# Kernel optimization log

Hardware: AMD Instinct MI355X
Metric: run time of the kernel (lower is better)

Reference implementation:

```python
import jax, jax.numpy as jnp
import numpy as np

NEG = -1.0e9  # matches torch's masked_fill value
EPS = 1e-12


def setup_inputs() -> dict:
    key = jax.random.key(0)
    ks = jax.random.split(key, 8)
    B, T, S, E, H, M = 128, 512, 512, 256, 1024, 4

    def lin_w(k, fan_in, fan_out):
        lim = 1.0 / np.sqrt(fan_in)
        return jax.random.uniform(k, (fan_in, fan_out), jnp.float32, -lim, lim)

    return {
        "state": jax.random.normal(ks[0], (B, S), jnp.float32),
        "task_features": jax.random.normal(ks[1], (B, T, 5), jnp.float32),
        "nest_ids": jax.random.randint(ks[2], (B, T), 0, M),
        "task_mask": jnp.ones((B, T), jnp.bool_),
        "emb_w": lin_w(ks[3], 5, E),
        "emb_b": jnp.zeros((E,), jnp.float32),
        "w1": lin_w(ks[4], S + E, H),
        "b1": jnp.zeros((H,), jnp.float32),
        "w2": lin_w(ks[5], H, H),
        "b2": jnp.zeros((H,), jnp.float32),
        "w3": lin_w(ks[6], H, 1),
        "b3": jnp.zeros((1,), jnp.float32),
        "etas": jnp.ones((M,), jnp.float32),  # eta_buf (learn_eta=False, eta_init=1.0)
    }


def reference(state, task_features, nest_ids, task_mask,
              emb_w, emb_b, w1, b1, w2, b2, w3, b3, etas):
    B, T, _ = task_features.shape
    M = etas.shape[0]

    # per-task utilities: MLP over concat(state, task_embed)  [B,T]
    te = task_features @ emb_w + emb_b                                # [B,T,E]
    x = jnp.concatenate(
        [jnp.broadcast_to(state[:, None, :], (B, T, state.shape[-1])), te], axis=-1)
    h = jax.nn.relu(x @ w1 + b1)
    h = jax.nn.relu(h @ w2 + b2)
    utils = (h @ w3 + b3)[..., 0]                                     # [B,T]
    utils = jnp.where(task_mask, utils, NEG)

    # nest membership masks (vectorized segment-softmax over nests)
    mem = (nest_ids[..., None] == jnp.arange(M)) & task_mask[..., None]  # [B,T,M]
    nonempty = mem.any(axis=1)                                           # [B,M]

    mval = jnp.max(jnp.where(mem, utils[..., None], -jnp.inf), axis=1)   # [B,M]
    mval = jnp.where(nonempty, mval, 0.0)
    scaled = (utils[..., None] - mval[:, None, :]) / etas                # [B,T,M]
    sums = jnp.sum(jnp.where(mem, jnp.exp(scaled), 0.0), axis=1)         # [B,M]

    # inclusive values U_m = mval + eta_m * log(sum exp((v-mval)/eta_m))
    U = jnp.where(nonempty, mval + etas * jnp.log(jnp.clip(sums, EPS)), NEG)
    p_nest = jax.nn.softmax(U, axis=-1)                                  # [B,M]

    # per-task within-nest probabilities, gathered via nest id
    nid = jnp.clip(nest_ids, 0, M - 1)
    m_t = jnp.take_along_axis(mval, nid, axis=1)                         # [B,T]
    s_t = jnp.take_along_axis(jnp.clip(sums, EPS), nid, axis=1)          # [B,T]
    pn_t = jnp.take_along_axis(p_nest, nid, axis=1)                      # [B,T]
    e_t = jnp.exp((utils - m_t) / etas[nid])
    valid = task_mask & (nest_ids >= 0) & (nest_ids < M)
    p_task = jnp.where(valid, pn_t * e_t / s_t, 0.0)                     # [B,T]

    # degenerate fallback: uniform over valid tasks when everything underflowed
    any_valid = task_mask.any(axis=1)
    fallback = any_valid & (p_task.sum(axis=1) <= EPS)
    uni = 1.0 / jnp.maximum(task_mask.sum(axis=1), 1).astype(p_task.dtype)
    p_task = jnp.where(fallback[:, None] & task_mask, uni[:, None], p_task)

    return utils, p_task, p_nest
```

## Files before the change

### kernel.cpp

```cpp
#include <hip/hip_runtime.h>
#include <stdint.h>

#define NEGV -1.0e9f
#define EPSV 1e-12f

typedef __attribute__((ext_vector_type(8))) short bf16x8;
typedef __attribute__((ext_vector_type(4))) float f32x4;

__device__ __forceinline__ unsigned int f2bf(float f) {
  unsigned int u = __builtin_bit_cast(unsigned int, f);
  u = u + 0x7FFFu + ((u >> 16) & 1u);
  return u >> 16;
}

__device__ __forceinline__ unsigned int cvt_pk_bf16(float lo, float hi) {
  unsigned int r;
  asm("v_cvt_pk_bf16_f32 %0, %1, %2" : "=v"(r) : "v"(lo), "v"(hi));
  return r;
}

__global__ __launch_bounds__(256) void k_prep(
    const float* __restrict__ state, const float* __restrict__ w1,
    const float* __restrict__ b1, const float* __restrict__ emb_w,
    const float* __restrict__ emb_b, const float* __restrict__ w2,
    float* __restrict__ W1e, float* __restrict__ sb,
    unsigned short* __restrict__ W2t) {
  const int blk = blockIdx.x;
  const int tid = threadIdx.x;
  if (blk < 4) {
    const int j = blk * 256 + tid;
    float a0 = 0.f, a1 = 0.f, a2 = 0.f, a3 = 0.f, a4 = 0.f;
    for (int e = 0; e < 256; ++e) {
      const float w = w1[(size_t)(512 + e) * 1024 + j];
      a0 += emb_w[0 * 256 + e] * w;
      a1 += emb_w[1 * 256 + e] * w;
      a2 += emb_w[2 * 256 + e] * w;
      a3 += emb_w[3 * 256 + e] * w;
      a4 += emb_w[4 * 256 + e] * w;
    }
    W1e[0 * 1024 + j] = a0;
    W1e[1 * 1024 + j] = a1;
    W1e[2 * 1024 + j] = a2;
    W1e[3 * 1024 + j] = a3;
    W1e[4 * 1024 + j] = a4;
  } else if (blk < 516) {
    const int blk2 = blk - 4;
    const int b = blk2 >> 2;
    const int j = (blk2 & 3) * 256 + tid;
    float acc = b1[j];
    for (int e = 0; e < 256; ++e)
      acc += emb_b[e] * w1[(size_t)(512 + e) * 1024 + j];
    const float* st = state + (size_t)b * 512;
    for (int s = 0; s < 512; ++s) acc += st[s] * w1[(size_t)s * 1024 + j];
    sb[(size_t)b * 1024 + j] = acc;
  } else {
    __shared__ float tile[64][65];
    const int blk2 = blk - 516;
    const int gn = blk2 & 15, gk = blk2 >> 4;
    const int c = tid & 63, w = tid >> 6;
#pragma unroll
    for (int i = 0; i < 16; ++i) {
      const int r = i * 4 + w;
      tile[r][c] = w2[(size_t)(gk * 64 + r) * 1024 + gn * 64 + c];
    }
    __syncthreads();
#pragma unroll
    for (int i = 0; i < 16; ++i) {
      const int r = i * 4 + w;
      W2t[(size_t)(gn * 64 + r) * 1024 + gk * 64 + c] = (unsigned short)f2bf(tile[c][r]);
    }
  }
}

__global__ __launch_bounds__(256) void k_h1(
    const float* __restrict__ tf, const float* __restrict__ sbm,
    const float* __restrict__ W1em, unsigned short* __restrict__ H1) {
  const int tid = threadIdx.x;
  const int j0 = (tid & 127) << 3;
  const int r0 = (blockIdx.x * 2 + (tid >> 7)) * 8;
  const int b = r0 >> 9;
  float ptf[8][5];
#pragma unroll
  for (int r = 0; r < 8; ++r) {
    const float* f = tf + (size_t)(r0 + r) * 5;
#pragma unroll
    for (int i = 0; i < 5; ++i) ptf[r][i] = f[i];
  }
  const float* sbp = sbm + (size_t)b * 1024 + j0;
  const float4 sa = *(const float4*)(sbp);
  const float4 sbv = *(const float4*)(sbp + 4);
  float4 wa[5], wb[5];
#pragma unroll
  for (int i = 0; i < 5; ++i) {
    wa[i] = *(const float4*)(W1em + i * 1024 + j0);
    wb[i] = *(const float4*)(W1em + i * 1024 + j0 + 4);
  }
#pragma unroll
  for (int r = 0; r < 8; ++r) {
    const float f0 = ptf[r][0], f1 = ptf[r][1], f2 = ptf[r][2],
                f3 = ptf[r][3], f4 = ptf[r][4];
    float h0 = fmaf(f4, wa[4].x, fmaf(f3, wa[3].x, fmaf(f2, wa[2].x, fmaf(f1, wa[1].x, fmaf(f0, wa[0].x, sa.x)))));
    float h1 = fmaf(f4, wa[4].y, fmaf(f3, wa[3].y, fmaf(f2, wa[2].y, fmaf(f1, wa[1].y, fmaf(f0, wa[0].y, sa.y)))));
    float h2 = fmaf(f4, wa[4].z, fmaf(f3, wa[3].z, fmaf(f2, wa[2].z, fmaf(f1, wa[1].z, fmaf(f0, wa[0].z, sa.z)))));
    float h3 = fmaf(f4, wa[4].w, fmaf(f3, wa[3].w, fmaf(f2, wa[2].w, fmaf(f1, wa[1].w, fmaf(f0, wa[0].w, sa.w)))));
    float h4 = fmaf(f4, wb[4].x, fmaf(f3, wb[3].x, fmaf(f2, wb[2].x, fmaf(f1, wb[1].x, fmaf(f0, wb[0].x, sbv.x)))));
    float h5 = fmaf(f4, wb[4].y, fmaf(f3, wb[3].y, fmaf(f2, wb[2].y, fmaf(f1, wb[1].y, fmaf(f0, wb[0].y, sbv.y)))));
    float h6 = fmaf(f4, wb[4].z, fmaf(f3, wb[3].z, fmaf(f2, wb[2].z, fmaf(f1, wb[1].z, fmaf(f0, wb[0].z, sbv.z)))));
    float h7 = fmaf(f4, wb[4].w, fmaf(f3, wb[3].w, fmaf(f2, wb[2].w, fmaf(f1, wb[1].w, fmaf(f0, wb[0].w, sbv.w)))));
    h0 = fmaxf(h0, 0.f); h1 = fmaxf(h1, 0.f); h2 = fmaxf(h2, 0.f); h3 = fmaxf(h3, 0.f);
    h4 = fmaxf(h4, 0.f); h5 = fmaxf(h5, 0.f); h6 = fmaxf(h6, 0.f); h7 = fmaxf(h7, 0.f);
    uint4 pk;
    pk.x = cvt_pk_bf16(h0, h1);
    pk.y = cvt_pk_bf16(h2, h3);
    pk.z = cvt_pk_bf16(h4, h5);
    pk.w = cvt_pk_bf16(h6, h7);
    *(uint4*)&H1[(size_t)(r0 + r) * 1024 + j0] = pk;
  }
}

__global__ __launch_bounds__(512, 2) void k_gemm2(
    const unsigned short* __restrict__ H1, const unsigned short* __restrict__ W2t,
    const float* __restrict__ b2, const float* __restrict__ w3,
    float* __restrict__ partial) {
  __shared__ unsigned short As[2][16384];
  __shared__ unsigned short Bs[2][16384];

  const int bid = blockIdx.x;
  const int swz = (bid & 7) * 128 + (bid >> 3);
  const int bx = swz >> 2, by = swz & 3;
  const int row0 = bx << 8, col0 = by << 8;

  const int tid = threadIdx.x, lane = tid & 63, wid = tid >> 6;

  const int sr = (wid << 5) + (lane >> 3);
  const int scol = (((lane & 7) ^ ((lane >> 3) & 7)) << 3);
  const size_t abase = (size_t)(row0 + sr) * 1024 + scol;
  const size_t bbase = (size_t)(col0 + sr) * 1024 + scol;
  const int ldsb = (wid << 5) * 64;

#define STAGE8(kt, d)                                                         \
    _Pragma("unroll")                                                         \
    for (int q = 0; q < 4; ++q) {                                             \
      __builtin_amdgcn_global_load_lds(                                       \
          (const __attribute__((address_space(1))) void*)(                    \
              H1 + abase + (size_t)q * 8192 + (kt) * 64),                     \
          (__attribute__((address_space(3))) void*)(As[d] + ldsb + q * 512),  \
          16, 0, 0);                                                          \
      __builtin_amdgcn_global_load_lds(                                       \
          (const __attribute__((address_space(1))) void*)(                    \
              W2t + bbase + (size_t)q * 8192 + (kt) * 64),                    \
          (__attribute__((address_space(3))) void*)(Bs[d] + ldsb + q * 512),  \
          16, 0, 0);                                                          \
    }

#define STAGE4(kt, d, g)                                                      \
    _Pragma("unroll")                                                         \
    for (int qq = 2 * (g); qq < 2 * (g) + 2; ++qq) {                          \
      __builtin_amdgcn_global_load_lds(                                       \
          (const __attribute__((address_space(1))) void*)(                    \
              H1 + abase + (size_t)qq * 8192 + (kt) * 64),                    \
          (__attribute__((address_space(3))) void*)(As[d] + ldsb + qq * 512), \
          16, 0, 0);                                                          \
      __builtin_amdgcn_global_load_lds(                                       \
          (const __attribute__((address_space(1))) void*)(                    \
              W2t + bbase + (size_t)qq * 8192 + (kt) * 64),                   \
          (__attribute__((address_space(3))) void*)(Bs[d] + ldsb + qq * 512), \
          16, 0, 0);                                                          \
    }

  const int wr = wid >> 2, wc = wid & 3;
  const int lm = lane & 15, lg = lane >> 4;
  const int aoff = (wr * 128 + lm) * 64;
  const int boff = (wc * 64 + lm) * 64;
  const int s0 = ((lg ^ (lm & 7)) << 3);
  const int s1 = (((4 + lg) ^ (lm & 7)) << 3);

  f32x4 acc[8][4];
#pragma unroll
  for (int m = 0; m < 8; ++m)
#pragma unroll
    for (int n = 0; n < 4; ++n) acc[m][n] = (f32x4){0.f, 0.f, 0.f, 0.f};

  STAGE8(0, 0);
  __syncthreads();

#pragma unroll 1
  for (int t = 0; t < 16; ++t) {
    const unsigned short* Ad = As[t & 1];
    const unsigned short* Bd = Bs[t & 1];
    bf16x8 bk0[4], bk1[4], aS[2][4];
#pragma unroll
    for (int n = 0; n < 4; ++n) {
      bk0[n] = *(const bf16x8*)(Bd + boff + n * 1024 + s0);
      bk1[n] = *(const bf16x8*)(Bd + boff + n * 1024 + s1);
    }
    aS[0][0] = *(const bf16x8*)(Ad + aoff + 0 * 1024 + s0);
    aS[0][1] = *(const bf16x8*)(Ad + aoff + 0 * 1024 + s1);
    aS[0][2] = *(const bf16x8*)(Ad + aoff + 1 * 1024 + s0);
    aS[0][3] = *(const bf16x8*)(Ad + aoff + 1 * 1024 + s1);
#pragma unroll
    for (int p = 0; p < 4; ++p) {
      const int cur = p & 1, nxt = cur ^ 1;
      if (p < 3) {
        aS[nxt][0] = *(const bf16x8*)(Ad + aoff + (2 * p + 2) * 1024 + s0);
        aS[nxt][1] = *(const bf16x8*)(Ad + aoff + (2 * p + 2) * 1024 + s1);
        aS[nxt][2] = *(const bf16x8*)(Ad + aoff + (2 * p + 3) * 1024 + s0);
        aS[nxt][3] = *(const bf16x8*)(Ad + aoff + (2 * p + 3) * 1024 + s1);
      }
      if (t < 15 && p < 2) STAGE4(t + 1, (t + 1) & 1, p);
      __builtin_amdgcn_s_barrier();
      __builtin_amdgcn_s_setprio(1);
#pragma unroll
      for (int n = 0; n < 4; ++n)
        acc[2 * p][n] = __builtin_amdgcn_mfma_f32_16x16x32_bf16(aS[cur][0], bk0[n], acc[2 * p][n], 0, 0, 0);
#pragma unroll
      for (int n = 0; n < 4; ++n)
        acc[2 * p][n] = __builtin_amdgcn_mfma_f32_16x16x32_bf16(aS[cur][1], bk1[n], acc[2 * p][n], 0, 0, 0);
#pragma unroll
      for (int n = 0; n < 4; ++n)
        acc[2 * p + 1][n] = __builtin_amdgcn_mfma_f32_16x16x32_bf16(aS[cur][2], bk0[n], acc[2 * p + 1][n], 0, 0, 0);
#pragma unroll
      for (int n = 0; n < 4; ++n)
        acc[2 * p + 1][n] = __builtin_amdgcn_mfma_f32_16x16x32_bf16(aS[cur][3], bk1[n], acc[2 * p + 1][n], 0, 0, 0);
      __builtin_amdgcn_s_setprio(0);
      if (p == 3 && t < 15) asm volatile("s_waitcnt vmcnt(0)" ::: "memory");
      __builtin_amdgcn_s_barrier();
    }
  }
#undef STAGE8
#undef STAGE4

  float b2v[4], w3v[4];
#pragma unroll
  for (int n = 0; n < 4; ++n) {
    const int col = col0 + wc * 64 + n * 16 + lm;
    b2v[n] = b2[col];
    w3v[n] = w3[col];
  }
#pragma unroll
  for (int m = 0; m < 8; ++m) {
#pragma unroll
    for (int r = 0; r < 4; ++r) {
      float v = 0.f;
#pragma unroll
      for (int n = 0; n < 4; ++n) {
        float h = acc[m][n][r] + b2v[n];
        h = fmaxf(h, 0.f);
        v += h * w3v[n];
      }
      v += __shfl_xor(v, 1, 16);
      v += __shfl_xor(v, 2, 16);
      v += __shfl_xor(v, 4, 16);
      v += __shfl_xor(v, 8, 16);
      if (lm == 0)
        partial[(size_t)(row0 + wr * 128 + m * 16 + lg * 4 + r) * 16 + by * 4 + wc] = v;
    }
  }
}

__global__ __launch_bounds__(512) void k_softmax(
    const float* __restrict__ partial, const float* __restrict__ b3,
    const int* __restrict__ nids, const int* __restrict__ mask,
    const float* __restrict__ etas, float* __restrict__ utils_out,
    float* __restrict__ p_task, float* __restrict__ p_nest) {
  const int b = blockIdx.x, tid = threadIdx.x;
  const int lane = tid & 63, wv = tid >> 6;
  __shared__ float smax[8][4];
  __shared__ int scnt[8][4];
  __shared__ float ssum[8][4];
  __shared__ float sred[8];
  __shared__ int sredi[8];

  const size_t base = (size_t)b * 512;
  const float b3v = b3[0];
  const size_t row = base + tid;
  const float4* p = (const float4*)(partial + row * 16);
  const float4 pa = p[0], pb = p[1], pc = p[2], pd = p[3];
  const float uraw = b3v + pa.x + pa.y + pa.z + pa.w + pb.x + pb.y + pb.z + pb.w +
                     pc.x + pc.y + pc.z + pc.w + pd.x + pd.y + pd.z + pd.w;
  const int n0 = nids[row];
  const bool m0 = mask[row] != 0;
  const float u0 = m0 ? uraw : NEGV;
  utils_out[row] = u0;
  const float eta[4] = {etas[0], etas[1], etas[2], etas[3]};

  float lmax[4]; int lcnt[4];
#pragma unroll
  for (int m = 0; m < 4; ++m) {
    const bool e0 = m0 && (n0 == m);
    lmax[m] = e0 ? u0 : -INFINITY;
    lcnt[m] = (int)e0;
  }
#pragma unroll
  for (int m = 0; m < 4; ++m)
#pragma unroll
    for (int off = 32; off >= 1; off >>= 1) {
      lmax[m] = fmaxf(lmax[m], __shfl_xor(lmax[m], off));
      lcnt[m] += __shfl_xor(lcnt[m], off);
    }
  if (lane == 0) {
#pragma unroll
    for (int m = 0; m < 4; ++m) { smax[wv][m] = lmax[m]; scnt[wv][m] = lcnt[m]; }
  }
  __syncthreads();
  float mval[4]; bool ne[4];
#pragma unroll
  for (int m = 0; m < 4; ++m) {
    float mx = smax[0][m];
    int c = scnt[0][m];
#pragma unroll
    for (int w = 1; w < 8; ++w) { mx = fmaxf(mx, smax[w][m]); c += scnt[w][m]; }
    ne[m] = c > 0;
    mval[m] = ne[m] ? mx : 0.f;
  }
  float lsum[4];
#pragma unroll
  for (int m = 0; m < 4; ++m)
    lsum[m] = (m0 && n0 == m) ? expf((u0 - mval[m]) / eta[m]) : 0.f;
#pragma unroll
  for (int m = 0; m < 4; ++m)
#pragma unroll
    for (int off = 32; off >= 1; off >>= 1) lsum[m] += __shfl_xor(lsum[m], off);
  if (lane == 0) {
#pragma unroll
    for (int m = 0; m < 4; ++m) ssum[wv][m] = lsum[m];
  }
  __syncthreads();
  float sums[4], U[4];
#pragma unroll
  for (int m = 0; m < 4; ++m) {
    float s = ssum[0][m];
#pragma unroll
    for (int w = 1; w < 8; ++w) s += ssum[w][m];
    sums[m] = fmaxf(s, EPSV);
    U[m] = ne[m] ? (mval[m] + eta[m] * logf(sums[m])) : NEGV;
  }
  const float mU = fmaxf(fmaxf(U[0], U[1]), fmaxf(U[2], U[3]));
  float pe[4], pes = 0.f;
#pragma unroll
  for (int m = 0; m < 4; ++m) { pe[m] = expf(U[m] - mU); pes += pe[m]; }
  float pn[4];
#pragma unroll
  for (int m = 0; m < 4; ++m) pn[m] = pe[m] / pes;
  if (tid == 0) {
#pragma unroll
    for (int m = 0; m < 4; ++m) p_nest[(size_t)b * 4 + m] = pn[m];
  }
  const bool valid = m0 && n0 >= 0 && n0 < 4;
  float mt = 0.f, st = 1.f, pnt = 0.f, et = 1.f;
#pragma unroll
  for (int m = 0; m < 4; ++m)
    if (n0 == m) { mt = mval[m]; st = sums[m]; pnt = pn[m]; et = eta[m]; }
  float pt = valid ? pnt * expf((u0 - mt) / et) / st : 0.f;

  float lp = pt;
  int lmk = (int)m0;
#pragma unroll
  for (int off = 32; off >= 1; off >>= 1) {
    lp += __shfl_xor(lp, off);
    lmk += __shfl_xor(lmk, off);
  }
  if (lane == 0) { sred[wv] = lp; sredi[wv] = lmk; }
  __syncthreads();
  float sumpt = sred[0];
  int nmask = sredi[0];
#pragma unroll
  for (int w = 1; w < 8; ++w) { sumpt += sred[w]; nmask += sredi[w]; }
  const bool fallback = (nmask > 0) && (sumpt <= EPSV);
  if (fallback) {
    const float uni = 1.f / (float)(nmask > 0 ? nmask : 1);
    pt = m0 ? uni : pt;
  }
  p_task[row] = pt;
}

extern "C" void kernel_launch(void* const* d_in, const int* in_sizes, int n_in,
                              void* d_out, int out_size, void* d_ws, size_t ws_size,
                              hipStream_t stream) {
  const float* state = (const float*)d_in[0];
  const float* tf = (const float*)d_in[1];
  const int* nids = (const int*)d_in[2];
  const int* mask = (const int*)d_in[3];
  const float* emb_w = (const float*)d_in[4];
  const float* emb_b = (const float*)d_in[5];
  const float* w1 = (const float*)d_in[6];
  const float* b1 = (const float*)d_in[7];
  const float* w2 = (const float*)d_in[8];
  const float* b2 = (const float*)d_in[9];
  const float* w3 = (const float*)d_in[10];
  const float* b3 = (const float*)d_in[11];
  const float* etas = (const float*)d_in[12];

  float* out = (float*)d_out;
  float* utils_out = out;
  float* p_task = out + 65536;
  float* p_nest = out + 131072;

  char* ws = (char*)d_ws;
  unsigned short* W2t = (unsigned short*)ws; ws += 1024ull * 1024 * 2;
  float* partial = (float*)ws;               ws += 65536ull * 16 * 4;
  float* W1e = (float*)ws;                   ws += 5 * 1024 * 4;
  float* sb = (float*)ws;                    ws += 128 * 1024 * 4;
  unsigned short* H1 = (unsigned short*)ws;  ws += 65536ull * 1024 * 2;

  k_prep<<<772, 256, 0, stream>>>(state, w1, b1, emb_w, emb_b, w2, W1e, sb, W2t);
  k_h1<<<4096, 256, 0, stream>>>(tf, sb, W1e, H1);
  k_gemm2<<<1024, 512, 0, stream>>>(H1, W2t, b2, w3, partial);
  k_softmax<<<128, 512, 0, stream>>>(partial, b3, nids, mask, etas,
                                     utils_out, p_task, p_nest);
}
```

Measured before the change: 181.7 us.

## Load GEMM2 A operand directly from global into registers, keep B in LDS

Stops staging the H1 (A) tile through shared memory in the second GEMM. Each wave now reads its A fragments straight from global memory into registers, prefetching them one sub-phase ahead, while only the W2 (B) tile is still double-buffered in LDS with async global-to-LDS loads. This halves LDS use and removes LDS reads and bank traffic for A. In exchange, the four waves that share a row group fetch the same A rows redundantly from global memory or cache, and A loads are narrower row-strided accesses whose latency must be hidden by the register prefetch.

Result: slower. 382.4 us (+110.4%).

```diff
diff --git a/kernel.cpp b/kernel.cpp
--- a/kernel.cpp
+++ b/kernel.cpp
@@ -122,7 +122,6 @@
     const unsigned short* __restrict__ H1, const unsigned short* __restrict__ W2t,
     const float* __restrict__ b2, const float* __restrict__ w3,
     float* __restrict__ partial) {
-  __shared__ unsigned short As[2][16384];
   __shared__ unsigned short Bs[2][16384];
 
   const int bid = blockIdx.x;
@@ -132,48 +131,25 @@
 
   const int tid = threadIdx.x, lane = tid & 63, wid = tid >> 6;
 
-  const int sr = (wid << 5) + (lane >> 3);
-  const int scol = (((lane & 7) ^ ((lane >> 3) & 7)) << 3);
-  const size_t abase = (size_t)(row0 + sr) * 1024 + scol;
-  const size_t bbase = (size_t)(col0 + sr) * 1024 + scol;
-  const int ldsb = (wid << 5) * 64;
-
-#define STAGE8(kt, d)                                                         \
+  const int bcol = (wid << 3) + (lane >> 3);
+  const int bscol = (((lane & 7) ^ ((lane >> 3) & 7)) << 3);
+
+#define STAGEB2(kt, g)                                                        \
     _Pragma("unroll")                                                         \
-    for (int q = 0; q < 4; ++q) {                                             \
+    for (int q = 2 * (g); q < 2 * (g) + 2; ++q) {                             \
       __builtin_amdgcn_global_load_lds(                                       \
           (const __attribute__((address_space(1))) void*)(                    \
-              H1 + abase + (size_t)q * 8192 + (kt) * 64),                     \
-          (__attribute__((address_space(3))) void*)(As[d] + ldsb + q * 512),  \
-          16, 0, 0);                                                          \
-      __builtin_amdgcn_global_load_lds(                                       \
-          (const __attribute__((address_space(1))) void*)(                    \
-              W2t + bbase + (size_t)q * 8192 + (kt) * 64),                    \
-          (__attribute__((address_space(3))) void*)(Bs[d] + ldsb + q * 512),  \
-          16, 0, 0);                                                          \
-    }
-
-#define STAGE4(kt, d, g)                                                      \
-    _Pragma("unroll")                                                         \
-    for (int qq = 2 * (g); qq < 2 * (g) + 2; ++qq) {                          \
-      __builtin_amdgcn_global_load_lds(                                       \
-          (const __attribute__((address_space(1))) void*)(                    \
-              H1 + abase + (size_t)qq * 8192 + (kt) * 64),                    \
-          (__attribute__((address_space(3))) void*)(As[d] + ldsb + qq * 512), \
-          16, 0, 0);                                                          \
-      __builtin_amdgcn_global_load_lds(                                       \
-          (const __attribute__((address_space(1))) void*)(                    \
-              W2t + bbase + (size_t)qq * 8192 + (kt) * 64),                   \
-          (__attribute__((address_space(3))) void*)(Bs[d] + ldsb + qq * 512), \
-          16, 0, 0);                                                          \
+              W2t + (size_t)(col0 + q * 64 + bcol) * 1024 + (kt) * 64 + bscol), \
+          (__attribute__((address_space(3))) void*)(                          \
+              Bs[(kt) & 1] + (q * 64 + (wid << 3)) * 64), 16, 0, 0);          \
     }
 
   const int wr = wid >> 2, wc = wid & 3;
   const int lm = lane & 15, lg = lane >> 4;
-  const int aoff = (wr * 128 + lm) * 64;
   const int boff = (wc * 64 + lm) * 64;
   const int s0 = ((lg ^ (lm & 7)) << 3);
   const int s1 = (((4 + lg) ^ (lm & 7)) << 3);
+  const unsigned short* aptr = H1 + (size_t)(row0 + wr * 128 + lm) * 1024 + lg * 8;
 
   f32x4 acc[8][4];
 #pragma unroll
@@ -181,54 +157,78 @@
 #pragma unroll
     for (int n = 0; n < 4; ++n) acc[m][n] = (f32x4){0.f, 0.f, 0.f, 0.f};
 
-  STAGE8(0, 0);
-  __syncthreads();
+  STAGEB2(0, 0);
+  STAGEB2(0, 1);
+  bf16x8 ANf[4], A1f[4], A0f[4];
+  ANf[0] = *(const bf16x8*)(aptr + 0);
+  ANf[1] = *(const bf16x8*)(aptr + 32);
+  ANf[2] = *(const bf16x8*)(aptr + 16384);
+  ANf[3] = *(const bf16x8*)(aptr + 16384 + 32);
+  asm volatile("s_waitcnt vmcnt(0)" ::: "memory");
+  __builtin_amdgcn_s_barrier();
+
+#define MFMA16(mp, F)                                                         \
+    _Pragma("unroll")                                                         \
+    for (int n = 0; n < 4; ++n)                                               \
+      acc[2 * (mp)][n] = __builtin_amdgcn_mfma_f32_16x16x32_bf16(F[0], bk0[n], acc[2 * (mp)][n], 0, 0, 0); \
+    _Pragma("unroll")                                                         \
+    for (int n = 0; n < 4; ++n)                                               \
+      acc[2 * (mp) + 1][n] = __builtin_amdgcn_mfma_f32_16x16x32_bf16(F[2], bk0[n], acc[2 * (mp) + 1][n], 0, 0, 0); \
+    _Pragma("unroll")                                                         \
+    for (int n = 0; n < 4; ++n)                                               \
+      acc[2 * (mp)][n] = __builtin_amdgcn_mfma_f32_16x16x32_bf16(F[1], bk1[n], acc[2 * (mp)][n], 0, 0, 0); \
+    _Pragma("unroll")                                                         \
+    for (int n = 0; n < 4; ++n)                                               \
+      acc[2 * (mp) + 1][n] = __builtin_amdgcn_mfma_f32_16x16x32_bf16(F[3], bk1[n], acc[2 * (mp) + 1][n], 0, 0, 0);
 
 #pragma unroll 1
   for (int t = 0; t < 16; ++t) {
-    const unsigned short* Ad = As[t & 1];
     const unsigned short* Bd = Bs[t & 1];
-    bf16x8 bk0[4], bk1[4], aS[2][4];
+    bf16x8 bk0[4], bk1[4];
 #pragma unroll
     for (int n = 0; n < 4; ++n) {
       bk0[n] = *(const bf16x8*)(Bd + boff + n * 1024 + s0);
       bk1[n] = *(const bf16x8*)(Bd + boff + n * 1024 + s1);
     }
-    aS[0][0] = *(const bf16x8*)(Ad + aoff + 0 * 1024 + s0);
-    aS[0][1] = *(const bf16x8*)(Ad + aoff + 0 * 1024 + s1);
-    aS[0][2] = *(const bf16x8*)(Ad + aoff + 1 * 1024 + s0);
-    aS[0][3] = *(const bf16x8*)(Ad + aoff + 1 * 1024 + s1);
-#pragma unroll
-    for (int p = 0; p < 4; ++p) {
-      const int cur = p & 1, nxt = cur ^ 1;
-      if (p < 3) {
-        aS[nxt][0] = *(const bf16x8*)(Ad + aoff + (2 * p + 2) * 1024 + s0);
-        aS[nxt][1] = *(const bf16x8*)(Ad + aoff + (2 * p + 2) * 1024 + s1);
-        aS[nxt][2] = *(const bf16x8*)(Ad + aoff + (2 * p + 3) * 1024 + s0);
-        aS[nxt][3] = *(const bf16x8*)(Ad + aoff + (2 * p + 3) * 1024 + s1);
-      }
-      if (t < 15 && p < 2) STAGE4(t + 1, (t + 1) & 1, p);
-      __builtin_amdgcn_s_barrier();
-      __builtin_amdgcn_s_setprio(1);
-#pragma unroll
-      for (int n = 0; n < 4; ++n)
-        acc[2 * p][n] = __builtin_amdgcn_mfma_f32_16x16x32_bf16(aS[cur][0], bk0[n], acc[2 * p][n], 0, 0, 0);
-#pragma unroll
-      for (int n = 0; n < 4; ++n)
-        acc[2 * p][n] = __builtin_amdgcn_mfma_f32_16x16x32_bf16(aS[cur][1], bk1[n], acc[2 * p][n], 0, 0, 0);
-#pragma unroll
-      for (int n = 0; n < 4; ++n)
-        acc[2 * p + 1][n] = __builtin_amdgcn_mfma_f32_16x16x32_bf16(aS[cur][2], bk0[n], acc[2 * p + 1][n], 0, 0, 0);
-#pragma unroll
-      for (int n = 0; n < 4; ++n)
-        acc[2 * p + 1][n] = __builtin_amdgcn_mfma_f32_16x16x32_bf16(aS[cur][3], bk1[n], acc[2 * p + 1][n], 0, 0, 0);
-      __builtin_amdgcn_s_setprio(0);
-      if (p == 3 && t < 15) asm volatile("s_waitcnt vmcnt(0)" ::: "memory");
-      __builtin_amdgcn_s_barrier();
-    }
-  }
-#undef STAGE8
-#undef STAGE4
+    A1f[0] = *(const bf16x8*)(aptr + 2 * 16384 + t * 64);
+    A1f[1] = *(const bf16x8*)(aptr + 2 * 16384 + t * 64 + 32);
+    A1f[2] = *(const bf16x8*)(aptr + 3 * 16384 + t * 64);
+    A1f[3] = *(const bf16x8*)(aptr + 3 * 16384 + t * 64 + 32);
+    if (t < 15) STAGEB2(t + 1, 0);
+    __builtin_amdgcn_s_setprio(1);
+    MFMA16(0, ANf);
+    __builtin_amdgcn_s_setprio(0);
+    __builtin_amdgcn_s_barrier();
+    A0f[0] = *(const bf16x8*)(aptr + 4 * 16384 + t * 64);
+    A0f[1] = *(const bf16x8*)(aptr + 4 * 16384 + t * 64 + 32);
+    A0f[2] = *(const bf16x8*)(aptr + 5 * 16384 + t * 64);
+    A0f[3] = *(const bf16x8*)(aptr + 5 * 16384 + t * 64 + 32);
+    if (t < 15) STAGEB2(t + 1, 1);
+    __builtin_amdgcn_s_setprio(1);
+    MFMA16(1, A1f);
+    __builtin_amdgcn_s_setprio(0);
+    __builtin_amdgcn_s_barrier();
+    A1f[0] = *(const bf16x8*)(aptr + 6 * 16384 + t * 64);
+    A1f[1] = *(const bf16x8*)(aptr + 6 * 16384 + t * 64 + 32);
+    A1f[2] = *(const bf16x8*)(aptr + 7 * 16384 + t * 64);
+    A1f[3] = *(const bf16x8*)(aptr + 7 * 16384 + t * 64 + 32);
+    if (t < 15) {
+      ANf[0] = *(const bf16x8*)(aptr + (t + 1) * 64);
+      ANf[1] = *(const bf16x8*)(aptr + (t + 1) * 64 + 32);
+      ANf[2] = *(const bf16x8*)(aptr + 16384 + (t + 1) * 64);
+      ANf[3] = *(const bf16x8*)(aptr + 16384 + (t + 1) * 64 + 32);
+    }
+    __builtin_amdgcn_s_setprio(1);
+    MFMA16(2, A0f);
+    __builtin_amdgcn_s_setprio(0);
+    __builtin_amdgcn_s_barrier();
+    __builtin_amdgcn_s_setprio(1);
+    MFMA16(3, A1f);
+    __builtin_amdgcn_s_setprio(0);
+    __builtin_amdgcn_s_barrier();
+  }
+#undef MFMA16
+#undef STAGEB2
 
   float b2v[4], w3v[4];
 #pragma unroll
```
